# Optimization experiments

Hardware: AMD Instinct MI355X
Metric: run time of the kernel (lower is better)

The kernel has to match this reference:

```python
import jax, jax.numpy as jnp
import numpy as np

EMBED = 1024
N_HEAD = 16
HEAD_DIM = EMBED // N_HEAD


def setup_inputs() -> dict:
    key = jax.random.key(0)
    ks = jax.random.split(key, 9)
    def xavier(k, shape, fan_in, fan_out):
        bound = float(np.sqrt(6.0 / (fan_in + fan_out)))
        return jax.random.uniform(k, shape, jnp.float32, -bound, bound)
    x = jax.random.normal(ks[0], (4, 2048, EMBED), jnp.float32)
    wq = xavier(ks[1], (N_HEAD, EMBED, HEAD_DIM), EMBED, HEAD_DIM)
    wk = xavier(ks[2], (N_HEAD, EMBED, HEAD_DIM), EMBED, HEAD_DIM)
    wv = xavier(ks[3], (N_HEAD, EMBED, HEAD_DIM), EMBED, HEAD_DIM)
    bq = jnp.zeros((N_HEAD, 1, HEAD_DIM), jnp.float32)
    bk = jnp.zeros((N_HEAD, 1, HEAD_DIM), jnp.float32)
    bv = jnp.zeros((N_HEAD, 1, HEAD_DIM), jnp.float32)
    # nn.Linear default init: uniform(-1/sqrt(in), 1/sqrt(in)), weight [out, in]
    bnd = 1.0 / float(np.sqrt(EMBED))
    wo = jax.random.uniform(ks[4], (EMBED, EMBED), jnp.float32, -bnd, bnd)
    bo = jax.random.uniform(ks[5], (EMBED,), jnp.float32, -bnd, bnd)
    return {"x": x, "wq": wq, "bq": bq, "wk": wk, "bk": bk,
            "wv": wv, "bv": bv, "wo": wo, "bo": bo}


def reference(x, wq, bq, wk, bk, wv, bv, wo, bo):
    # per-head projections: [b,s,d] x [h,d,e] -> [b,h,s,e]
    q = jnp.einsum('bsd,hde->bhse', x, wq) + bq
    k = jnp.einsum('bsd,hde->bhse', x, wk) + bk
    v = jnp.einsum('bsd,hde->bhse', x, wv) + bv
    scale = 1.0 / jnp.sqrt(jnp.asarray(q.shape[-1], q.dtype))
    scores = jax.nn.softmax(jnp.einsum('bhse,bhte->bhst', q, k) * scale, axis=-1)
    att = jnp.einsum('bhst,bhte->bhse', scores, v)  # [b,h,s,e]
    b, h, s, e = att.shape
    att = att.transpose(0, 2, 1, 3).reshape(b, s, h * e)
    return att @ wo.T + bo
```

## Files before the change

### kernel.cpp

```cpp
#include <hip/hip_runtime.h>
#include <hip/hip_bf16.h>
#include <stdint.h>

typedef __attribute__((ext_vector_type(8))) short short8;
typedef __attribute__((ext_vector_type(4))) short short4v;
typedef __attribute__((ext_vector_type(4))) float f32x4;
typedef __attribute__((ext_vector_type(4))) float float4v;

#define LOG2E_OVER8 0.18033688011112042f

__device__ __forceinline__ short bf16r(float f) {
  union { float f; uint32_t u; } v; v.f = f;
  uint32_t r = (v.u + 0x7FFFu + ((v.u >> 16) & 1u)) >> 16;
  return (short)r;
}

__device__ __forceinline__ void gload16(const void* g, void* l) {
  __builtin_amdgcn_global_load_lds((const __attribute__((address_space(1))) void*)g,
                                   (__attribute__((address_space(3))) void*)l, 16, 0, 0);
}

__global__ void k_prep(const float* __restrict__ x, const float* __restrict__ wo,
                       const float* __restrict__ wq, const float* __restrict__ wk,
                       const float* __restrict__ wv,
                       short* __restrict__ xb, short* __restrict__ wob,
                       short* __restrict__ wt) {
  __shared__ short tile[64][65];
  int bid = blockIdx.x;
  int tid = threadIdx.x;
  if (bid < 8192) {
    int i = bid * 256 + tid;
    float4v v = *(const float4v*)(x + (size_t)i * 4);
    short4v o = { bf16r(v[0]), bf16r(v[1]), bf16r(v[2]), bf16r(v[3]) };
    *(short4v*)(xb + (size_t)i * 4) = o;
  } else if (bid < 9216) {
    int i = (bid - 8192) * 256 + tid;
    float4v v = *(const float4v*)(wo + (size_t)i * 4);
    short4v o = { bf16r(v[0]), bf16r(v[1]), bf16r(v[2]), bf16r(v[3]) };
    *(short4v*)(wob + (size_t)i * 4) = o;
  } else {
    int b2 = bid - 9216;
    int kt = b2 & 15, h = (b2 >> 4) & 15, wsel = b2 >> 8;
    const float* src = wsel == 0 ? wq : (wsel == 1 ? wk : wv);
    {
      int e = tid & 63, r4 = tid >> 6;
#pragma unroll
      for (int p = 0; p < 16; ++p) {
        int kk = p * 4 + r4;
        tile[kk][e] = bf16r(src[h * 65536 + (kt * 64 + kk) * 64 + e]);
      }
    }
    __syncthreads();
    {
      int kk = tid & 63, r4 = tid >> 6;
#pragma unroll
      for (int p = 0; p < 16; ++p) {
        int e = p * 4 + r4;
        wt[(size_t)(wsel * 1024 + h * 64 + e) * 1024 + kt * 64 + kk] = tile[kk][e];
      }
    }
  }
}

template<int EPI>
__global__ __launch_bounds__(256, 2) void k_gemm(
    const short* __restrict__ A, const short* __restrict__ Bt,
    const float* __restrict__ b0, const float* __restrict__ b1, const float* __restrict__ b2,
    short* __restrict__ qb, short* __restrict__ kb, short* __restrict__ vtb,
    float* __restrict__ outp) {
  __shared__ short smem[36864];
  int tid = threadIdx.x;
  int l = tid & 63, w = tid >> 6;
  int g = l >> 4, c = l & 15;
  int wr = w >> 1, wc = w & 1;
  const int NBX = (EPI == 0) ? 24 : 8;
  const int nwg = NBX * 32;
  int orig = blockIdx.x + blockIdx.y * NBX;
  int swz = (orig & 7) * (nwg >> 3) + (orig >> 3);
  int m0 = (swz / NBX) * 256, n0 = (swz % NBX) * 128;

  f32x4 acc[8][4];
#pragma unroll
  for (int i = 0; i < 8; ++i)
#pragma unroll
    for (int j = 0; j < 4; ++j) acc[i][j] = (f32x4){0.f, 0.f, 0.f, 0.f};

  int aoff[8], boff[4];
#pragma unroll
  for (int mi = 0; mi < 8; ++mi) {
    int R = wr * 128 + mi * 16 + c;
    aoff[mi] = R * 32 + ((g ^ ((R >> 1) & 3)) * 8);
  }
#pragma unroll
  for (int ni = 0; ni < 4; ++ni) {
    int R = wc * 64 + ni * 16 + c;
    boff[ni] = R * 32 + ((g ^ ((R >> 1) & 3)) * 8);
  }

  const short* asrc[4]; int adst[4];
  const short* bsrc[2]; int bdst[2];
#pragma unroll
  for (int i = 0; i < 4; ++i) {
    int ch = i * 256 + tid;
    int row = ch >> 2, cbs = ch & 3;
    int sb = cbs ^ ((row >> 1) & 3);
    asrc[i] = A + (size_t)(m0 + row) * 1024 + sb * 8;
    adst[i] = ch * 8;
  }
#pragma unroll
  for (int i = 0; i < 2; ++i) {
    int ch = i * 256 + tid;
    int row = ch >> 2, cbs = ch & 3;
    int sb = cbs ^ ((row >> 1) & 3);
    bsrc[i] = Bt + (size_t)(n0 + row) * 1024 + sb * 8;
    bdst[i] = ch * 8;
  }

#pragma unroll
  for (int i = 0; i < 4; ++i) gload16(asrc[i], &smem[adst[i]]);
#pragma unroll
  for (int i = 0; i < 2; ++i) gload16(bsrc[i], &smem[24576 + bdst[i]]);
#pragma unroll
  for (int i = 0; i < 4; ++i) gload16(asrc[i] + 32, &smem[8192 + adst[i]]);
#pragma unroll
  for (int i = 0; i < 2; ++i) gload16(bsrc[i] + 32, &smem[24576 + 4096 + bdst[i]]);
  asm volatile("s_waitcnt vmcnt(6)" ::: "memory");
  __builtin_amdgcn_s_barrier();

  int cur = 0;
  for (int kt = 0; kt < 32; ++kt) {
    int stg = cur + 2; if (stg >= 3) stg -= 3;
    const short* Ab = &smem[cur * 8192];
    const short* Bb = &smem[24576 + cur * 4096];
    bool pre = (kt + 2 < 32);
    int ko = (kt + 2) * 32;

    short8 af0[4], bf[4];
#pragma unroll
    for (int mi = 0; mi < 4; ++mi) af0[mi] = *(const short8*)&Ab[aoff[mi]];
#pragma unroll
    for (int ni = 0; ni < 4; ++ni) bf[ni] = *(const short8*)&Bb[boff[ni]];
    if (pre) {
      gload16(asrc[0] + ko, &smem[stg * 8192 + adst[0]]);
      gload16(asrc[1] + ko, &smem[stg * 8192 + adst[1]]);
      gload16(bsrc[0] + ko, &smem[24576 + stg * 4096 + bdst[0]]);
    }
    __builtin_amdgcn_s_setprio(1);
#pragma unroll
    for (int mi = 0; mi < 4; ++mi)
#pragma unroll
      for (int ni = 0; ni < 4; ++ni)
        acc[mi][ni] = __builtin_amdgcn_mfma_f32_16x16x32_bf16(af0[mi], bf[ni], acc[mi][ni], 0, 0, 0);
    __builtin_amdgcn_s_setprio(0);

    short8 af1[4];
#pragma unroll
    for (int mi = 0; mi < 4; ++mi) af1[mi] = *(const short8*)&Ab[aoff[mi + 4]];
    if (pre) {
      gload16(asrc[2] + ko, &smem[stg * 8192 + adst[2]]);
      gload16(asrc[3] + ko, &smem[stg * 8192 + adst[3]]);
      gload16(bsrc[1] + ko, &smem[24576 + stg * 4096 + bdst[1]]);
    }
    __builtin_amdgcn_s_setprio(1);
#pragma unroll
    for (int mi = 0; mi < 4; ++mi)
#pragma unroll
      for (int ni = 0; ni < 4; ++ni)
        acc[mi + 4][ni] = __builtin_amdgcn_mfma_f32_16x16x32_bf16(af1[mi], bf[ni], acc[mi + 4][ni], 0, 0, 0);
    __builtin_amdgcn_s_setprio(0);

    if (kt < 31) {
      if (kt < 30) asm volatile("s_waitcnt vmcnt(6)" ::: "memory");
      else         asm volatile("s_waitcnt vmcnt(0)" ::: "memory");
      __builtin_amdgcn_s_barrier();
    }
    cur = cur + 1; if (cur == 3) cur = 0;
  }

  if (EPI == 0 && n0 >= 2048) {
    __syncthreads();
#pragma unroll
    for (int mi = 0; mi < 8; ++mi)
#pragma unroll
      for (int ni = 0; ni < 4; ++ni) {
        int ln = wc * 64 + ni * 16 + c;
        float bias = b2[(n0 - 2048) + ln];
        int ls0 = wr * 128 + mi * 16 + g * 4;
        int blk = ls0 >> 3;
        int sblk = blk ^ (ln & 31);
        short4v o;
#pragma unroll
        for (int r = 0; r < 4; ++r) o[r] = bf16r(acc[mi][ni][r] + bias);
        *(short4v*)&smem[ln * 256 + sblk * 8 + (ls0 & 7)] = o;
      }
    __syncthreads();
    int b = m0 >> 11, s0g = m0 & 2047;
    int h0 = (n0 - 2048) >> 6;
    int vrow0 = (b * 16 + h0) * 64;
#pragma unroll
    for (int p = 0; p < 16; ++p) {
      int ln = p * 8 + (tid >> 5);
      int L2 = tid & 31;
      int T = L2 >> 3, B = L2 & 7;
      int sa0 = T * 64 + (B >> 2) * 32 + (B & 3) * 4;
      int sb0 = sa0 + 16;
      short4v va = *(const short4v*)&smem[ln * 256 + ((sa0 >> 3) ^ (ln & 31)) * 8 + (sa0 & 7)];
      short4v vb = *(const short4v*)&smem[ln * 256 + ((sb0 >> 3) ^ (ln & 31)) * 8 + (sb0 & 7)];
      short8 v = {va[0], va[1], va[2], va[3], vb[0], vb[1], vb[2], vb[3]};
      *(short8*)&vtb[(size_t)(vrow0 + ln) * 2048 + s0g + L2 * 8] = v;
    }
    return;
  }

#pragma unroll
  for (int mi = 0; mi < 8; ++mi)
#pragma unroll
    for (int ni = 0; ni < 4; ++ni) {
      int n = n0 + wc * 64 + ni * 16 + c;
      if (EPI == 0) {
        int sel = n >> 10, nn = n & 1023;
        int h = nn >> 6, e = nn & 63;
        const float* bp = sel == 0 ? b0 : b1;
        short* dst = sel == 0 ? qb : kb;
        float bias = bp[nn];
        float sc = (sel == 0) ? LOG2E_OVER8 : 1.0f;
#pragma unroll
        for (int r = 0; r < 4; ++r) {
          int m = m0 + wr * 128 + mi * 16 + g * 4 + r;
          int b = m >> 11, s = m & 2047;
          float v = (acc[mi][ni][r] + bias) * sc;
          dst[(size_t)((b * 16 + h) * 2048 + s) * 64 + e] = bf16r(v);
        }
      } else {
        float bias = b0[n];
#pragma unroll
        for (int r = 0; r < 4; ++r) {
          int m = m0 + wr * 128 + mi * 16 + g * 4 + r;
          outp[(size_t)m * 1024 + n] = acc[mi][ni][r] + bias;
        }
      }
    }
}

__global__ __launch_bounds__(256, 4) void k_attn(
    const short* __restrict__ Qb, const short* __restrict__ Kb,
    const short* __restrict__ Vt, short* __restrict__ attb) {
  __shared__ short Ks[2][64 * 64];
  __shared__ short Vs[2][64 * 64];
  int tid = threadIdx.x;
  int l = tid & 63, w = tid >> 6;
  int g = l >> 4, c = l & 15;
  int orig = blockIdx.x + blockIdx.y * 16;
  int swz = (orig & 7) * 128 + (orig >> 3);
  int qt = swz & 15, bh = swz >> 4;
  int q0 = qt * 128 + w * 32;

  const short* Qh = Qb + (size_t)bh * 2048 * 64;
  short8 qf[2][2];
#pragma unroll
  for (int qi = 0; qi < 2; ++qi)
#pragma unroll
    for (int es = 0; es < 2; ++es)
      qf[qi][es] = *(const short8*)&Qh[(size_t)(q0 + qi * 16 + c) * 64 + es * 32 + g * 8];

  int koff[4][2];
#pragma unroll
  for (int mi = 0; mi < 4; ++mi) {
    int row = mi * 16 + c;
    koff[mi][0] = row * 64 + ((g ^ (row & 7)) * 8);
    koff[mi][1] = row * 64 + (((4 + g) ^ (row & 7)) * 8);
  }
  int voff[2][4];
#pragma unroll
  for (int ks = 0; ks < 2; ++ks)
#pragma unroll
    for (int ei = 0; ei < 4; ++ei) {
      int row = ei * 16 + c;
      voff[ks][ei] = row * 64 + (((ks * 4 + g) ^ (row & 7)) * 8);
    }

  const short* kptr[2];
  const short* vptr[2];
  int ldst[2];
#pragma unroll
  for (int i = 0; i < 2; ++i) {
    int ch = w * 128 + i * 64 + l;
    int row = ch >> 3, cbs = ch & 7;
    int sb = cbs ^ (row & 7);
    kptr[i] = Kb + (size_t)(bh * 2048 + row) * 64 + sb * 8;
    vptr[i] = Vt + (size_t)(bh * 64 + row) * 2048 + sb * 8;
    ldst[i] = (w * 128 + i * 64) * 8;
  }

  const f32x4 z4 = (f32x4){0.f, 0.f, 0.f, 0.f};
  f32x4 oacc[4][2];
#pragma unroll
  for (int i = 0; i < 4; ++i) { oacc[i][0] = z4; oacc[i][1] = z4; }
  f32x4 lsum[2] = {z4, z4};

  const short one_bf16 = (short)0x3F80;
  const short8 ones = {one_bf16, one_bf16, one_bf16, one_bf16,
                       one_bf16, one_bf16, one_bf16, one_bf16};

  auto stageKV = [&](int buf) {
#pragma unroll
    for (int i = 0; i < 2; ++i) {
      gload16(kptr[i], &Ks[buf][ldst[i]]);
      gload16(vptr[i], &Vs[buf][ldst[i]]);
      kptr[i] += 64 * 64;
      vptr[i] += 64;
    }
  };

  stageKV(0);
  __syncthreads();

  for (int t = 0; t < 32; ++t) {
    int buf = t & 1;
    if (t + 1 < 32) stageKV(buf ^ 1);

    const short* Kbuf = &Ks[buf][0];
    short8 kf0[4], kf1[4];
#pragma unroll
    for (int mi = 0; mi < 4; ++mi) {
      kf0[mi] = *(const short8*)&Kbuf[koff[mi][0]];
      kf1[mi] = *(const short8*)&Kbuf[koff[mi][1]];
    }
    f32x4 sacc[4][2];
    __builtin_amdgcn_s_setprio(1);
#pragma unroll
    for (int mi = 0; mi < 4; ++mi)
#pragma unroll
      for (int qi = 0; qi < 2; ++qi)
        sacc[mi][qi] = __builtin_amdgcn_mfma_f32_16x16x32_bf16(kf0[mi], qf[qi][0], z4, 0, 0, 0);
#pragma unroll
    for (int mi = 0; mi < 4; ++mi)
#pragma unroll
      for (int qi = 0; qi < 2; ++qi)
        sacc[mi][qi] = __builtin_amdgcn_mfma_f32_16x16x32_bf16(kf1[mi], qf[qi][1], sacc[mi][qi], 0, 0, 0);
    __builtin_amdgcn_s_setprio(0);

    short8 pf[2][2];
#pragma unroll
    for (int qi = 0; qi < 2; ++qi) {
      float p[4][4];
#pragma unroll
      for (int mi = 0; mi < 4; ++mi)
#pragma unroll
        for (int r = 0; r < 4; ++r)
          p[mi][r] = __builtin_amdgcn_exp2f(sacc[mi][qi][r]);
#pragma unroll
      for (int ks = 0; ks < 2; ++ks) {
        union { uint32_t w[4]; short8 s; } pu;
        asm("v_cvt_pk_bf16_f32 %0, %1, %2" : "=v"(pu.w[0]) : "v"(p[ks * 2][0]), "v"(p[ks * 2][1]));
        asm("v_cvt_pk_bf16_f32 %0, %1, %2" : "=v"(pu.w[1]) : "v"(p[ks * 2][2]), "v"(p[ks * 2][3]));
        asm("v_cvt_pk_bf16_f32 %0, %1, %2" : "=v"(pu.w[2]) : "v"(p[ks * 2 + 1][0]), "v"(p[ks * 2 + 1][1]));
        asm("v_cvt_pk_bf16_f32 %0, %1, %2" : "=v"(pu.w[3]) : "v"(p[ks * 2 + 1][2]), "v"(p[ks * 2 + 1][3]));
        pf[qi][ks] = pu.s;
      }
    }

    const short* Vbuf = &Vs[buf][0];
    __builtin_amdgcn_s_setprio(1);
#pragma unroll
    for (int qi = 0; qi < 2; ++qi)
#pragma unroll
      for (int ks = 0; ks < 2; ++ks)
        lsum[qi] = __builtin_amdgcn_mfma_f32_16x16x32_bf16(ones, pf[qi][ks], lsum[qi], 0, 0, 0);
#pragma unroll
    for (int ks = 0; ks < 2; ++ks)
#pragma unroll
      for (int ei = 0; ei < 4; ++ei) {
        short8 vf = *(const short8*)&Vbuf[voff[ks][ei]];
#pragma unroll
        for (int qi = 0; qi < 2; ++qi)
          oacc[ei][qi] = __builtin_amdgcn_mfma_f32_16x16x32_bf16(vf, pf[qi][ks], oacc[ei][qi], 0, 0, 0);
      }
    __builtin_amdgcn_s_setprio(0);

    __syncthreads();
  }

  int b = bh >> 4, h = bh & 15;
#pragma unroll
  for (int qi = 0; qi < 2; ++qi) {
    float inv = 1.0f / lsum[qi][0];
    int s = q0 + qi * 16 + c;
#pragma unroll
    for (int ei = 0; ei < 4; ++ei) {
      short4v o;
#pragma unroll
      for (int r = 0; r < 4; ++r) o[r] = bf16r(oacc[ei][qi][r] * inv);
      *(short4v*)&attb[(size_t)(b * 2048 + s) * 1024 + h * 64 + ei * 16 + g * 4] = o;
    }
  }
}

extern "C" void kernel_launch(void* const* d_in, const int* in_sizes, int n_in,
                              void* d_out, int out_size, void* d_ws, size_t ws_size,
                              hipStream_t stream) {
  const float* x  = (const float*)d_in[0];
  const float* wq = (const float*)d_in[1];
  const float* bq = (const float*)d_in[2];
  const float* wk = (const float*)d_in[3];
  const float* bk = (const float*)d_in[4];
  const float* wv = (const float*)d_in[5];
  const float* bv = (const float*)d_in[6];
  const float* wo = (const float*)d_in[7];
  const float* bo = (const float*)d_in[8];
  float* out = (float*)d_out;

  uint8_t* ws = (uint8_t*)d_ws;
  short* xb  = (short*)(ws);
  short* wt  = (short*)(ws + (16u << 20));
  short* wob = (short*)(ws + (22u << 20));
  short* qb  = (short*)(ws + (24u << 20));
  short* kb  = (short*)(ws + (40u << 20));
  short* vtb = (short*)(ws + (56u << 20));
  short* attb = xb;

  k_prep<<<9984, 256, 0, stream>>>(x, wo, wq, wk, wv, xb, wob, wt);
  k_gemm<0><<<dim3(24, 32), 256, 0, stream>>>(xb, wt, bq, bk, bv, qb, kb, vtb, nullptr);
  k_attn<<<dim3(16, 64), 256, 0, stream>>>(qb, kb, vtb, attb);
  k_gemm<1><<<dim3(8, 32), 256, 0, stream>>>(attb, wob, bo, nullptr, nullptr,
                                             nullptr, nullptr, nullptr, out);
}
```

Baseline: 161.8 us.

## Use 8 waves and BK=64 K-tiles in the projection GEMMs

The GEMM kernels move from 256 to 512 threads (8 waves, each owning a 64x64 sub-tile instead of 128x64) and double the K-tile depth from 32 to 64, which halves the number of loop iterations and barriers. LDS usage doubles to 144 KB per block, and the swizzle is changed to an 8-chunk XOR pattern. The goal is more waves to hide latency and fewer synchronisations per K. The cost is higher LDS pressure, which may limit residency to one block per CU despite the launch bound of 2, and each wave now loads its B fragments twice per iteration.

```diff
diff --git a/kernel.cpp b/kernel.cpp
--- a/kernel.cpp
+++ b/kernel.cpp
@@ -63,12 +63,12 @@
 }
 
 template<int EPI>
-__global__ __launch_bounds__(256, 2) void k_gemm(
+__global__ __launch_bounds__(512, 2) void k_gemm(
     const short* __restrict__ A, const short* __restrict__ Bt,
     const float* __restrict__ b0, const float* __restrict__ b1, const float* __restrict__ b2,
     short* __restrict__ qb, short* __restrict__ kb, short* __restrict__ vtb,
     float* __restrict__ outp) {
-  __shared__ short smem[36864];
+  __shared__ short smem[73728];
   int tid = threadIdx.x;
   int l = tid & 63, w = tid >> 6;
   int g = l >> 4, c = l & 15;
@@ -79,39 +79,43 @@
   int swz = (orig & 7) * (nwg >> 3) + (orig >> 3);
   int m0 = (swz / NBX) * 256, n0 = (swz % NBX) * 128;
 
-  f32x4 acc[8][4];
-#pragma unroll
-  for (int i = 0; i < 8; ++i)
+  f32x4 acc[4][4];
+#pragma unroll
+  for (int i = 0; i < 4; ++i)
 #pragma unroll
     for (int j = 0; j < 4; ++j) acc[i][j] = (f32x4){0.f, 0.f, 0.f, 0.f};
 
-  int aoff[8], boff[4];
-#pragma unroll
-  for (int mi = 0; mi < 8; ++mi) {
-    int R = wr * 128 + mi * 16 + c;
-    aoff[mi] = R * 32 + ((g ^ ((R >> 1) & 3)) * 8);
+  int aoff[4][2], boff[4][2];
+#pragma unroll
+  for (int mi = 0; mi < 4; ++mi) {
+    int R = wr * 64 + mi * 16 + c;
+#pragma unroll
+    for (int ks = 0; ks < 2; ++ks)
+      aoff[mi][ks] = R * 64 + (((ks * 4 + g) ^ (R & 7)) * 8);
   }
 #pragma unroll
   for (int ni = 0; ni < 4; ++ni) {
     int R = wc * 64 + ni * 16 + c;
-    boff[ni] = R * 32 + ((g ^ ((R >> 1) & 3)) * 8);
+#pragma unroll
+    for (int ks = 0; ks < 2; ++ks)
+      boff[ni][ks] = R * 64 + (((ks * 4 + g) ^ (R & 7)) * 8);
   }
 
   const short* asrc[4]; int adst[4];
   const short* bsrc[2]; int bdst[2];
 #pragma unroll
   for (int i = 0; i < 4; ++i) {
-    int ch = i * 256 + tid;
-    int row = ch >> 2, cbs = ch & 3;
-    int sb = cbs ^ ((row >> 1) & 3);
+    int ch = i * 512 + tid;
+    int row = ch >> 3, cbs = ch & 7;
+    int sb = cbs ^ (row & 7);
     asrc[i] = A + (size_t)(m0 + row) * 1024 + sb * 8;
     adst[i] = ch * 8;
   }
 #pragma unroll
   for (int i = 0; i < 2; ++i) {
-    int ch = i * 256 + tid;
-    int row = ch >> 2, cbs = ch & 3;
-    int sb = cbs ^ ((row >> 1) & 3);
+    int ch = i * 512 + tid;
+    int row = ch >> 3, cbs = ch & 7;
+    int sb = cbs ^ (row & 7);
     bsrc[i] = Bt + (size_t)(n0 + row) * 1024 + sb * 8;
     bdst[i] = ch * 8;
   }
@@ -119,58 +123,60 @@
 #pragma unroll
   for (int i = 0; i < 4; ++i) gload16(asrc[i], &smem[adst[i]]);
 #pragma unroll
-  for (int i = 0; i < 2; ++i) gload16(bsrc[i], &smem[24576 + bdst[i]]);
-#pragma unroll
-  for (int i = 0; i < 4; ++i) gload16(asrc[i] + 32, &smem[8192 + adst[i]]);
-#pragma unroll
-  for (int i = 0; i < 2; ++i) gload16(bsrc[i] + 32, &smem[24576 + 4096 + bdst[i]]);
+  for (int i = 0; i < 2; ++i) gload16(bsrc[i], &smem[49152 + bdst[i]]);
+#pragma unroll
+  for (int i = 0; i < 4; ++i) gload16(asrc[i] + 64, &smem[16384 + adst[i]]);
+#pragma unroll
+  for (int i = 0; i < 2; ++i) gload16(bsrc[i] + 64, &smem[49152 + 8192 + bdst[i]]);
   asm volatile("s_waitcnt vmcnt(6)" ::: "memory");
   __builtin_amdgcn_s_barrier();
 
   int cur = 0;
-  for (int kt = 0; kt < 32; ++kt) {
+  for (int kt = 0; kt < 16; ++kt) {
     int stg = cur + 2; if (stg >= 3) stg -= 3;
-    const short* Ab = &smem[cur * 8192];
-    const short* Bb = &smem[24576 + cur * 4096];
-    bool pre = (kt + 2 < 32);
-    int ko = (kt + 2) * 32;
-
-    short8 af0[4], bf[4];
-#pragma unroll
-    for (int mi = 0; mi < 4; ++mi) af0[mi] = *(const short8*)&Ab[aoff[mi]];
-#pragma unroll
-    for (int ni = 0; ni < 4; ++ni) bf[ni] = *(const short8*)&Bb[boff[ni]];
+    const short* Ab = &smem[cur * 16384];
+    const short* Bb = &smem[49152 + cur * 8192];
+    bool pre = (kt + 2 < 16);
+    int ko = (kt + 2) * 64;
+
+    short8 af0[4], bf0[4];
+#pragma unroll
+    for (int mi = 0; mi < 4; ++mi) af0[mi] = *(const short8*)&Ab[aoff[mi][0]];
+#pragma unroll
+    for (int ni = 0; ni < 4; ++ni) bf0[ni] = *(const short8*)&Bb[boff[ni][0]];
     if (pre) {
-      gload16(asrc[0] + ko, &smem[stg * 8192 + adst[0]]);
-      gload16(asrc[1] + ko, &smem[stg * 8192 + adst[1]]);
-      gload16(bsrc[0] + ko, &smem[24576 + stg * 4096 + bdst[0]]);
+      gload16(asrc[0] + ko, &smem[stg * 16384 + adst[0]]);
+      gload16(asrc[1] + ko, &smem[stg * 16384 + adst[1]]);
+      gload16(bsrc[0] + ko, &smem[49152 + stg * 8192 + bdst[0]]);
     }
     __builtin_amdgcn_s_setprio(1);
 #pragma unroll
     for (int mi = 0; mi < 4; ++mi)
 #pragma unroll
       for (int ni = 0; ni < 4; ++ni)
-        acc[mi][ni] = __builtin_amdgcn_mfma_f32_16x16x32_bf16(af0[mi], bf[ni], acc[mi][ni], 0, 0, 0);
+        acc[mi][ni] = __builtin_amdgcn_mfma_f32_16x16x32_bf16(af0[mi], bf0[ni], acc[mi][ni], 0, 0, 0);
     __builtin_amdgcn_s_setprio(0);
 
-    short8 af1[4];
-#pragma unroll
-    for (int mi = 0; mi < 4; ++mi) af1[mi] = *(const short8*)&Ab[aoff[mi + 4]];
+    short8 af1[4], bf1[4];
+#pragma unroll
+    for (int mi = 0; mi < 4; ++mi) af1[mi] = *(const short8*)&Ab[aoff[mi][1]];
+#pragma unroll
+    for (int ni = 0; ni < 4; ++ni) bf1[ni] = *(const short8*)&Bb[boff[ni][1]];
     if (pre) {
-      gload16(asrc[2] + ko, &smem[stg * 8192 + adst[2]]);
-      gload16(asrc[3] + ko, &smem[stg * 8192 + adst[3]]);
-      gload16(bsrc[1] + ko, &smem[24576 + stg * 4096 + bdst[1]]);
+      gload16(asrc[2] + ko, &smem[stg * 16384 + adst[2]]);
+      gload16(asrc[3] + ko, &smem[stg * 16384 + adst[3]]);
+      gload16(bsrc[1] + ko, &smem[49152 + stg * 8192 + bdst[1]]);
     }
     __builtin_amdgcn_s_setprio(1);
 #pragma unroll
     for (int mi = 0; mi < 4; ++mi)
 #pragma unroll
       for (int ni = 0; ni < 4; ++ni)
-        acc[mi + 4][ni] = __builtin_amdgcn_mfma_f32_16x16x32_bf16(af1[mi], bf[ni], acc[mi + 4][ni], 0, 0, 0);
+        acc[mi][ni] = __builtin_amdgcn_mfma_f32_16x16x32_bf16(af1[mi], bf1[ni], acc[mi][ni], 0, 0, 0);
     __builtin_amdgcn_s_setprio(0);
 
-    if (kt < 31) {
-      if (kt < 30) asm volatile("s_waitcnt vmcnt(6)" ::: "memory");
+    if (kt < 15) {
+      if (kt < 14) asm volatile("s_waitcnt vmcnt(6)" ::: "memory");
       else         asm volatile("s_waitcnt vmcnt(0)" ::: "memory");
       __builtin_amdgcn_s_barrier();
     }
@@ -180,12 +186,12 @@
   if (EPI == 0 && n0 >= 2048) {
     __syncthreads();
 #pragma unroll
-    for (int mi = 0; mi < 8; ++mi)
+    for (int mi = 0; mi < 4; ++mi)
 #pragma unroll
       for (int ni = 0; ni < 4; ++ni) {
         int ln = wc * 64 + ni * 16 + c;
         float bias = b2[(n0 - 2048) + ln];
-        int ls0 = wr * 128 + mi * 16 + g * 4;
+        int ls0 = wr * 64 + mi * 16 + g * 4;
         int blk = ls0 >> 3;
         int sblk = blk ^ (ln & 31);
         short4v o;
@@ -198,8 +204,8 @@
     int h0 = (n0 - 2048) >> 6;
     int vrow0 = (b * 16 + h0) * 64;
 #pragma unroll
-    for (int p = 0; p < 16; ++p) {
-      int ln = p * 8 + (tid >> 5);
+    for (int p = 0; p < 8; ++p) {
+      int ln = p * 16 + (tid >> 5);
       int L2 = tid & 31;
       int T = L2 >> 3, B = L2 & 7;
       int sa0 = T * 64 + (B >> 2) * 32 + (B & 3) * 4;
@@ -213,7 +219,7 @@
   }
 
 #pragma unroll
-  for (int mi = 0; mi < 8; ++mi)
+  for (int mi = 0; mi < 4; ++mi)
 #pragma unroll
     for (int ni = 0; ni < 4; ++ni) {
       int n = n0 + wc * 64 + ni * 16 + c;
@@ -226,7 +232,7 @@
         float sc = (sel == 0) ? LOG2E_OVER8 : 1.0f;
 #pragma unroll
         for (int r = 0; r < 4; ++r) {
-          int m = m0 + wr * 128 + mi * 16 + g * 4 + r;
+          int m = m0 + wr * 64 + mi * 16 + g * 4 + r;
           int b = m >> 11, s = m & 2047;
           float v = (acc[mi][ni][r] + bias) * sc;
           dst[(size_t)((b * 16 + h) * 2048 + s) * 64 + e] = bf16r(v);
@@ -235,7 +241,7 @@
         float bias = b0[n];
 #pragma unroll
         for (int r = 0; r < 4; ++r) {
-          int m = m0 + wr * 128 + mi * 16 + g * 4 + r;
+          int m = m0 + wr * 64 + mi * 16 + g * 4 + r;
           outp[(size_t)m * 1024 + n] = acc[mi][ni][r] + bias;
         }
       }
@@ -420,8 +426,8 @@
   short* attb = xb;
 
   k_prep<<<9984, 256, 0, stream>>>(x, wo, wq, wk, wv, xb, wob, wt);
-  k_gemm<0><<<dim3(24, 32), 256, 0, stream>>>(xb, wt, bq, bk, bv, qb, kb, vtb, nullptr);
+  k_gemm<0><<<dim3(24, 32), 512, 0, stream>>>(xb, wt, bq, bk, bv, qb, kb, vtb, nullptr);
   k_attn<<<dim3(16, 64), 256, 0, stream>>>(qb, kb, vtb, attb);
-  k_gemm<1><<<dim3(8, 32), 256, 0, stream>>>(attb, wob, bo, nullptr, nullptr,
+  k_gemm<1><<<dim3(8, 32), 512, 0, stream>>>(attb, wob, bo, nullptr, nullptr,
                                              nullptr, nullptr, nullptr, out);
 }
```

Result: faster. 156.6 us (-3.2%).
